# Kernel tuning notes

Hardware: AMD Instinct MI355X
Metric: run time of the kernel (lower is better)

## Reference

```python
import jax, jax.numpy as jnp
import numpy as np

# Fixed problem sizes (single FPN level, stride 8, 1280x1280 image)
N, A, C, H, W = 8, 1, 80, 160, 160
L = H * W * A
STRIDE = 8
IMG_SIZE = H * STRIDE
PRE_NMS_THRESH = 0.05
PRE_NMS_TOP_N = 1000
NMS_THRESH = 0.6
POST_TOP_N = 100
MIN_SIZE = 0.0
BBOX_XFORM_CLIP = float(np.log(1000.0 / 16.0))
TO_REMOVE = 1.0


def setup_inputs() -> dict:
    key = jax.random.key(0)
    k1, k2, k3 = jax.random.split(key, 3)
    box_regression = jax.random.normal(k1, (N, A * 4, H, W), jnp.float32)
    centerness = jax.random.normal(k2, (N, A, H, W), jnp.float32)
    box_cls = jax.random.normal(k3, (N, A * C, H, W), jnp.float32)
    # Anchor grid (one 8*stride/2-sized square anchor per location, shared across images)
    ys, xs = jnp.meshgrid(jnp.arange(H, dtype=jnp.float32), jnp.arange(W, dtype=jnp.float32), indexing="ij")
    cx = (xs.reshape(-1) + 0.5) * STRIDE
    cy = (ys.reshape(-1) + 0.5) * STRIDE
    half = 4.0 * STRIDE
    anchors = jnp.stack([cx - half, cy - half, cx + half, cy + half], axis=-1)  # [L,4] xyxy
    return {"box_regression": box_regression, "centerness": centerness, "box_cls": box_cls, "anchors": anchors}


def _flatten(x, c):
    # permute_and_flatten: [N, A*c, H, W] -> [N, H*W*A, c]
    return x.reshape(N, A, c, H, W).transpose(0, 3, 4, 1, 2).reshape(N, L, c)


def _decode(rel, anch):
    # ATSS BoxCoder.decode with weights (10,10,5,5)
    wx, wy, ww, wh = 10.0, 10.0, 5.0, 5.0
    widths = anch[:, 2] - anch[:, 0] + TO_REMOVE
    heights = anch[:, 3] - anch[:, 1] + TO_REMOVE
    ctr_x = anch[:, 0] + 0.5 * widths
    ctr_y = anch[:, 1] + 0.5 * heights
    dx = rel[:, 0] / wx
    dy = rel[:, 1] / wy
    dw = jnp.minimum(rel[:, 2] / ww, BBOX_XFORM_CLIP)
    dh = jnp.minimum(rel[:, 3] / wh, BBOX_XFORM_CLIP)
    pcx = dx * widths + ctr_x
    pcy = dy * heights + ctr_y
    pw = jnp.exp(dw) * widths
    ph = jnp.exp(dh) * heights
    return jnp.stack([pcx - 0.5 * (pw - TO_REMOVE), pcy - 0.5 * (ph - TO_REMOVE),
                      pcx + 0.5 * (pw - TO_REMOVE), pcy + 0.5 * (ph - TO_REMOVE)], axis=-1)


def _pairwise_iou(b):
    area = jnp.clip(b[:, 2] - b[:, 0], 0) * jnp.clip(b[:, 3] - b[:, 1], 0)
    lt = jnp.maximum(b[:, None, :2], b[None, :, :2])
    rb = jnp.minimum(b[:, None, 2:], b[None, :, 2:])
    wh = jnp.clip(rb - lt, 0)
    inter = wh[..., 0] * wh[..., 1]
    return inter / (area[:, None] + area[None, :] - inter + 1e-9)


def _per_image(scores, regression, cand, anchors):
    # scores [L,C] (already * centerness), cand [L,C] bool (thresholded BEFORE centerness)
    flat = jnp.where(cand, scores, -jnp.inf).reshape(-1)  # [L*C]
    vals, idx = jax.lax.top_k(flat, PRE_NMS_TOP_N)        # fixed-size pre-NMS topk
    loc = idx // C
    cls = idx % C + 1                                     # labels are 1-based
    valid = jnp.isfinite(vals)
    boxes = _decode(regression[loc], anchors[loc])
    x1 = jnp.clip(boxes[:, 0], 0.0, IMG_SIZE - 1.0)
    y1 = jnp.clip(boxes[:, 1], 0.0, IMG_SIZE - 1.0)
    x2 = jnp.clip(boxes[:, 2], 0.0, IMG_SIZE - 1.0)
    y2 = jnp.clip(boxes[:, 3], 0.0, IMG_SIZE - 1.0)
    boxes = jnp.stack([x1, y1, x2, y2], axis=-1)
    valid = valid & ((x2 - x1 + TO_REMOVE) >= MIN_SIZE) & ((y2 - y1 + TO_REMOVE) >= MIN_SIZE)
    sc = jnp.where(valid, jnp.sqrt(jnp.where(valid, vals, 1.0)), 0.0)
    # class-aware greedy NMS (boxlist_ml_nms): offset boxes by class so classes never overlap
    order = jnp.argsort(-jnp.where(valid, sc, -1.0))
    boxes, sc, cls, valid = boxes[order], sc[order], cls[order], valid[order]
    shifted = boxes + cls.astype(boxes.dtype)[:, None] * (4.0 * IMG_SIZE)
    iou = jax.lax.stop_gradient(_pairwise_iou(shifted))
    tri = jnp.triu(jnp.ones((PRE_NMS_TOP_N, PRE_NMS_TOP_N), bool), 1)
    iou = jnp.where(tri, iou, 0.0)

    def body(i, sup):
        keep_i = valid[i] & ~sup[i]
        return jnp.where(keep_i, sup | (iou[i] > NMS_THRESH), sup)

    sup = jax.lax.fori_loop(0, PRE_NMS_TOP_N, body, jnp.zeros(PRE_NMS_TOP_N, bool))
    keep = valid & ~sup
    fs = jnp.where(keep, sc, -1.0)
    topv, topi = jax.lax.top_k(fs, POST_TOP_N)            # fpn_post_nms_top_n cap
    ok = topv > 0
    out_boxes = jnp.where(ok[:, None], boxes[topi], 0.0)
    out_scores = jnp.where(ok, topv, 0.0)
    out_labels = jnp.where(ok, cls[topi], 0)
    dets = jnp.concatenate([out_boxes, out_scores[:, None]], axis=-1)  # [POST_TOP_N, 5]
    return dets, out_labels


def reference(box_regression, centerness, box_cls, anchors):
    cls_prob = jax.nn.sigmoid(_flatten(box_cls, C))                 # [N,L,C]
    ctr = jax.nn.sigmoid(_flatten(centerness, 1).reshape(N, L))     # [N,L]
    reg = _flatten(box_regression, 4)                               # [N,L,4]
    cand = cls_prob > PRE_NMS_THRESH                                # mask computed pre-centerness
    scores = cls_prob * ctr[:, :, None]
    dets, labels = jax.vmap(lambda s, r, c: _per_image(s, r, c, anchors))(scores, reg, cand)
    return dets, labels
```

## Files before the change

### kernel.cpp

```cpp
#include <hip/hip_runtime.h>
#include <cstdint>

static constexpr int NI   = 8;
static constexpr int CC   = 80;
static constexpr int LL   = 25600;
static constexpr int PRE_K  = 1000;
static constexpr int POST_K = 100;
static constexpr int HSIZE  = 2048;
static constexpr int CPCH   = 16;
static constexpr int NCH    = 5;
static constexpr int LPB    = 1024;
static constexpr int LBLK   = 25;
static constexpr int BPI    = NCH * LBLK;
static constexpr int CAPS   = 49152;
static constexpr int CAPFB  = 16384;
static constexpr int CAP2   = 8192;
static constexpr int BUFC   = 1024;
static constexpr float PRE_T = 0.05f;
static constexpr float NMS_T = 0.6f;
static constexpr float BSTAT = 0.65f;
static constexpr float XPRE  = 0.619f;
static constexpr uint32_t FBASE = 0x3F000000u;
static constexpr float CLIPV = 4.135166556742356f;
static constexpr float IMGM1 = 1279.0f;

__device__ __forceinline__ float sigm(float x) { return 1.0f / (1.0f + expf(-x)); }

__global__ __launch_bounds__(256) void k_scan(const float* __restrict__ cls,
                                              const float* __restrict__ ctr,
                                              uint32_t* __restrict__ cntS,
                                              uint32_t* __restrict__ ovf,
                                              unsigned long long* __restrict__ candS) {
    __shared__ unsigned long long sbuf[BUFC];
    __shared__ uint32_t s_cnt, s_base;
    const int t = threadIdx.x;
    if (t == 0) s_cnt = 0;
    __syncthreads();
    const int blk = blockIdx.x;
    const int n = blk / BPI, rem = blk % BPI, ch = rem / LBLK, lb = rem % LBLK;
    const int l0 = lb * LPB + t * 4;
    const uint32_t bstat = __float_as_uint(BSTAT);
    const float4 cr = *(const float4*)&ctr[(size_t)n * LL + l0];
    const float cv[4] = { sigm(cr.x), sigm(cr.y), sigm(cr.z), sigm(cr.w) };
    const float* base = cls + ((size_t)n * CC + ch * CPCH) * LL + l0;
#pragma unroll 1
    for (int cc0 = 0; cc0 < CPCH; cc0 += 4) {
        const float4 x0 = *(const float4*)&base[(size_t)(cc0 + 0) * LL];
        const float4 x1 = *(const float4*)&base[(size_t)(cc0 + 1) * LL];
        const float4 x2 = *(const float4*)&base[(size_t)(cc0 + 2) * LL];
        const float4 x3 = *(const float4*)&base[(size_t)(cc0 + 3) * LL];
        const float4 xs[4] = { x0, x1, x2, x3 };
#pragma unroll
        for (int u = 0; u < 4; ++u) {
            const float xv[4] = { xs[u].x, xs[u].y, xs[u].z, xs[u].w };
#pragma unroll
            for (int k = 0; k < 4; ++k) {
                if (xv[k] > XPRE) {
                    const float p = sigm(xv[k]);
                    if (p > PRE_T) {
                        const uint32_t bits = __float_as_uint(p * cv[k]);
                        if (bits >= bstat) {
                            uint32_t pos = atomicAdd(&s_cnt, 1u);
                            if (pos < (uint32_t)BUFC) {
                                uint32_t idx = (uint32_t)(l0 + k) * CC
                                             + (uint32_t)(ch * CPCH + cc0 + u);
                                sbuf[pos] = ((unsigned long long)bits << 32)
                                          | (uint32_t)(~idx);
                            }
                        }
                    }
                }
            }
        }
    }
    __syncthreads();
    if (t == 0) {
        s_base = atomicAdd(&cntS[n], s_cnt);
        if (s_cnt > (uint32_t)BUFC || s_base + s_cnt > (uint32_t)CAPS)
            atomicOr(&ovf[n], 1u);
    }
    __syncthreads();
    const uint32_t wr = min(s_cnt, (uint32_t)BUFC);
    const uint32_t b = s_base;
    if (b < (uint32_t)CAPS) {
        const uint32_t w = min(wr, (uint32_t)CAPS - b);
        for (uint32_t i = t; i < w; i += 256)
            candS[(size_t)n * CAPS + b + i] = sbuf[i];
    }
}

__global__ __launch_bounds__(256) void k_hist2(const unsigned long long* __restrict__ candS,
                                               const uint32_t* __restrict__ cntS,
                                               uint32_t* __restrict__ ghist2) {
    __shared__ uint32_t h[HSIZE];
    const int t = threadIdx.x;
    const int n = blockIdx.x >> 3, sub = blockIdx.x & 7;
    for (int i = t; i < HSIZE; i += 256) h[i] = 0u;
    __syncthreads();
    const uint32_t cnt = min(cntS[n], (uint32_t)CAPS);
    for (uint32_t i = (uint32_t)(sub * 256 + t); i < cnt; i += 2048) {
        const uint32_t bits = (uint32_t)(candS[(size_t)n * CAPS + i] >> 32);
        const uint32_t idx = min(2047u, (bits - FBASE) >> 12);
        atomicAdd(&h[idx], 1u);
    }
    __syncthreads();
    for (int b = t; b < HSIZE; b += 256)
        if (h[b]) atomicAdd(&ghist2[n * HSIZE + b], h[b]);
}

__global__ __launch_bounds__(256) void k_thresh2(const uint32_t* __restrict__ ghist2,
                                                 const uint32_t* __restrict__ cntS,
                                                 const uint32_t* __restrict__ ovf,
                                                 uint32_t* __restrict__ thr2,
                                                 uint32_t* __restrict__ listlen,
                                                 uint32_t* __restrict__ flag) {
    __shared__ uint32_t h[HSIZE];
    __shared__ uint32_t chunk[256];
    const int n = blockIdx.x, t = threadIdx.x;
    for (int b = t; b < HSIZE; b += 256) h[b] = ghist2[n * HSIZE + b];
    __syncthreads();
    uint32_t s = 0;
    for (int k = 0; k < 8; ++k) s += h[t * 8 + k];
    chunk[t] = s;
    __syncthreads();
    if (t == 0) {
        uint32_t cum = 0, nsel = 0;
        int T2 = -1;
        for (int c = 255; c >= 0 && T2 < 0; --c) {
            if (cum + chunk[c] >= (uint32_t)PRE_K) {
                for (int b = c * 8 + 7; b >= c * 8; --b) {
                    cum += h[b];
                    if (cum >= (uint32_t)PRE_K) { T2 = b; nsel = cum; break; }
                }
            } else cum += chunk[c];
        }
        const uint32_t tb = FBASE + ((uint32_t)max(T2, 0) << 12);
        thr2[n] = tb;
        listlen[n] = min(cntS[n], (uint32_t)CAPS);
        flag[n] = (T2 >= 0 && tb >= __float_as_uint(BSTAT) && !ovf[n] &&
                   nsel <= (uint32_t)CAP2) ? 1u : 0u;
    }
}

__global__ __launch_bounds__(256) void k_fbhist(const float* __restrict__ cls,
                                                const float* __restrict__ ctr,
                                                const uint32_t* __restrict__ flag,
                                                uint32_t* __restrict__ ghistC) {
    const int blk = blockIdx.x;
    const int n = blk / BPI;
    if (flag[n]) return;
    __shared__ uint32_t h[4][HSIZE];
    const int t = threadIdx.x;
    for (int i = t; i < 4 * HSIZE; i += 256) (&h[0][0])[i] = 0u;
    __syncthreads();
    const int rem = blk % BPI, ch = rem / LBLK, lb = rem % LBLK;
    const int l0 = lb * LPB + t * 4;
    const float4 cr = *(const float4*)&ctr[(size_t)n * LL + l0];
    const float cv[4] = { sigm(cr.x), sigm(cr.y), sigm(cr.z), sigm(cr.w) };
    uint32_t* hw = h[t >> 6];
    const float* base = cls + ((size_t)n * CC + ch * CPCH) * LL + l0;
#pragma unroll 1
    for (int cc = 0; cc < CPCH; ++cc) {
        const float4 x = *(const float4*)&base[(size_t)cc * LL];
        const float pv[4] = { sigm(x.x), sigm(x.y), sigm(x.z), sigm(x.w) };
#pragma unroll
        for (int k = 0; k < 4; ++k)
            if (pv[k] > PRE_T)
                atomicAdd(&hw[__float_as_uint(pv[k] * cv[k]) >> 19], 1u);
    }
    __syncthreads();
    for (int b = t; b < HSIZE; b += 256) {
        const uint32_t s = h[0][b] + h[1][b] + h[2][b] + h[3][b];
        if (s) atomicAdd(&ghistC[n * HSIZE + b], s);
    }
}

__global__ __launch_bounds__(256) void k_fbthresh(const uint32_t* __restrict__ ghistC,
                                                  const uint32_t* __restrict__ flag,
                                                  uint32_t* __restrict__ thr2) {
    const int n = blockIdx.x;
    if (flag[n]) return;
    __shared__ uint32_t h[HSIZE];
    __shared__ uint32_t chunk[256];
    const int t = threadIdx.x;
    for (int b = t; b < HSIZE; b += 256) h[b] = ghistC[n * HSIZE + b];
    __syncthreads();
    uint32_t s = 0;
    for (int k = 0; k < 8; ++k) s += h[t * 8 + k];
    chunk[t] = s;
    __syncthreads();
    if (t == 0) {
        uint32_t cum = 0;
        int T = 0;
        for (int c = 255; c >= 0; --c) {
            if (cum + chunk[c] >= (uint32_t)PRE_K) {
                for (int b = c * 8 + 7; b >= c * 8; --b) {
                    cum += h[b];
                    if (cum >= (uint32_t)PRE_K) { T = b; break; }
                }
                break;
            }
            cum += chunk[c];
        }
        thr2[n] = ((uint32_t)T) << 19;
    }
}

__global__ __launch_bounds__(256) void k_fbcollect(const float* __restrict__ cls,
                                                   const float* __restrict__ ctr,
                                                   const uint32_t* __restrict__ flag,
                                                   const uint32_t* __restrict__ thr2,
                                                   uint32_t* __restrict__ cntFB,
                                                   unsigned long long* __restrict__ candFB) {
    const int blk = blockIdx.x;
    const int n = blk / BPI;
    if (flag[n]) return;
    const int t = threadIdx.x;
    const int rem = blk % BPI, ch = rem / LBLK, lb = rem % LBLK;
    const int l0 = lb * LPB + t * 4;
    const uint32_t th = thr2[n];
    const float4 cr = *(const float4*)&ctr[(size_t)n * LL + l0];
    const float cv[4] = { sigm(cr.x), sigm(cr.y), sigm(cr.z), sigm(cr.w) };
    const float* base = cls + ((size_t)n * CC + ch * CPCH) * LL + l0;
#pragma unroll 1
    for (int cc = 0; cc < CPCH; ++cc) {
        const float4 x = *(const float4*)&base[(size_t)cc * LL];
        const float pv[4] = { sigm(x.x), sigm(x.y), sigm(x.z), sigm(x.w) };
#pragma unroll
        for (int k = 0; k < 4; ++k) {
            if (pv[k] > PRE_T) {
                const uint32_t bits = __float_as_uint(pv[k] * cv[k]);
                if (bits >= th) {
                    uint32_t pos = atomicAdd(&cntFB[n], 1u);
                    if (pos < (uint32_t)CAPFB) {
                        uint32_t idx = (uint32_t)(l0 + k) * CC + (uint32_t)(ch * CPCH + cc);
                        candFB[(size_t)n * CAPFB + pos] =
                            ((unsigned long long)bits << 32) | (uint32_t)(~idx);
                    }
                }
            }
        }
    }
}

__global__ __launch_bounds__(1024) void k_sortnms(const unsigned long long* __restrict__ candS,
                                                  const uint32_t* __restrict__ listlen,
                                                  const unsigned long long* __restrict__ candFB,
                                                  const uint32_t* __restrict__ cntFB,
                                                  unsigned long long* __restrict__ cand2,
                                                  const uint32_t* __restrict__ thr2,
                                                  const uint32_t* __restrict__ flag,
                                                  const float* __restrict__ reg,
                                                  const float* __restrict__ anch,
                                                  float* __restrict__ out) {
    __shared__ unsigned long long buf[2048];
    __shared__ float bx0[PRE_K], bx1[PRE_K], bx2[PRE_K], bx3[PRE_K];
    __shared__ float ar[PRE_K], scv[PRE_K];
    __shared__ int clsA[PRE_K], sup[PRE_K];
    __shared__ uint32_t s_cnt;
    __shared__ int s_kept;
    __shared__ int s_list[POST_K];
    const int n = blockIdx.x, t = threadIdx.x;
    if (t == 0) { s_cnt = 0; s_kept = 0; }
    __syncthreads();

    const bool fp = (flag[n] != 0);
    const unsigned long long* src = fp ? (candS + (size_t)n * CAPS)
                                       : (candFB + (size_t)n * CAPFB);
    const uint32_t len = fp ? listlen[n] : min(cntFB[n], (uint32_t)CAPFB);
    const unsigned long long Tkey = ((unsigned long long)thr2[n]) << 32;
    for (uint32_t gi = t; gi < len; gi += 1024) {
        const unsigned long long key = src[gi];
        if (key >= Tkey) {
            uint32_t pos = atomicAdd(&s_cnt, 1u);
            if (pos < (uint32_t)CAP2) cand2[(size_t)n * CAP2 + pos] = key;
        }
    }
    __syncthreads();
    const uint32_t M = min(s_cnt, (uint32_t)CAP2);

    buf[t]        = ((uint32_t)t < M)          ? cand2[(size_t)n * CAP2 + t]        : 0ULL;
    buf[1024 + t] = ((uint32_t)(1024 + t) < M) ? cand2[(size_t)n * CAP2 + 1024 + t] : 0ULL;
    for (uint32_t s = 0;;) {
        for (int k = 2; k <= 2048; k <<= 1) {
            for (int j = k >> 1; j > 0; j >>= 1) {
                __syncthreads();
#pragma unroll
                for (int u = 0; u < 2; ++u) {
                    const int i = t + u * 1024;
                    const int ixj = i ^ j;
                    if (ixj > i) {
                        const unsigned long long a = buf[i], b = buf[ixj];
                        const bool desc = ((i & k) == 0);
                        if (desc ? (a < b) : (a > b)) { buf[i] = b; buf[ixj] = a; }
                    }
                }
            }
        }
        __syncthreads();
        s = (s == 0) ? 2048 : s + 1024;
        if (s >= M) break;
        buf[1024 + t] = (s + t < M) ? cand2[(size_t)n * CAP2 + s + t] : 0ULL;
        __syncthreads();
    }

    if (t < PRE_K) {
        const unsigned long long key = buf[t];
        if (key == 0ULL) {
            sup[t] = 2; clsA[t] = -1;
            bx0[t] = bx1[t] = bx2[t] = bx3[t] = 0.0f; ar[t] = 0.0f; scv[t] = 0.0f;
        } else {
            const uint32_t bits = (uint32_t)(key >> 32);
            const uint32_t idx = ~(uint32_t)key;
            const int l = (int)(idx / (uint32_t)CC);
            const int c = (int)(idx % (uint32_t)CC);
            const float4 a = *(const float4*)&anch[l * 4];
            const float r0 = reg[((size_t)n * 4 + 0) * LL + l];
            const float r1 = reg[((size_t)n * 4 + 1) * LL + l];
            const float r2 = reg[((size_t)n * 4 + 2) * LL + l];
            const float r3 = reg[((size_t)n * 4 + 3) * LL + l];
            const float w  = a.z - a.x + 1.0f;
            const float h  = a.w - a.y + 1.0f;
            const float cx = a.x + 0.5f * w;
            const float cy = a.y + 0.5f * h;
            const float dx = r0 / 10.0f, dy = r1 / 10.0f;
            const float dw = fminf(r2 / 5.0f, CLIPV), dh = fminf(r3 / 5.0f, CLIPV);
            const float pcx = dx * w + cx, pcy = dy * h + cy;
            const float pw = expf(dw) * w, ph = expf(dh) * h;
            float x1 = pcx - 0.5f * (pw - 1.0f);
            float y1 = pcy - 0.5f * (ph - 1.0f);
            float x2 = pcx + 0.5f * (pw - 1.0f);
            float y2 = pcy + 0.5f * (ph - 1.0f);
            x1 = fminf(fmaxf(x1, 0.0f), IMGM1);
            y1 = fminf(fmaxf(y1, 0.0f), IMGM1);
            x2 = fminf(fmaxf(x2, 0.0f), IMGM1);
            y2 = fminf(fmaxf(y2, 0.0f), IMGM1);
            bx0[t] = x1; bx1[t] = y1; bx2[t] = x2; bx3[t] = y2;
            ar[t] = fmaxf(x2 - x1, 0.0f) * fmaxf(y2 - y1, 0.0f);
            scv[t] = sqrtf(__uint_as_float(bits));
            clsA[t] = c + 1;
            sup[t] = 0;
        }
    }
    __syncthreads();

    for (int i = 0; i < PRE_K; ++i) {
        if (s_kept >= POST_K) break;
        if (sup[i] == 0) {
            if (t == 0) s_list[s_kept] = i;
            if (t > i && t < PRE_K && sup[t] == 0 && clsA[t] == clsA[i]) {
                const float xx1 = fmaxf(bx0[i], bx0[t]);
                const float yy1 = fmaxf(bx1[i], bx1[t]);
                const float xx2 = fminf(bx2[i], bx2[t]);
                const float yy2 = fminf(bx3[i], bx3[t]);
                const float iw = fmaxf(xx2 - xx1, 0.0f);
                const float ih = fmaxf(yy2 - yy1, 0.0f);
                const float inter = iw * ih;
                const float iou = inter / (ar[i] + ar[t] - inter + 1e-9f);
                if (iou > NMS_T) sup[t] = 1;
            }
            if (t == 0) s_kept = s_kept + 1;
        }
        __syncthreads();
    }
    __syncthreads();

    if (t < POST_K) {
        float o0 = 0.f, o1 = 0.f, o2 = 0.f, o3 = 0.f, o4 = 0.f, lab = 0.f;
        if (t < s_kept) {
            const int i = s_list[t];
            o0 = bx0[i]; o1 = bx1[i]; o2 = bx2[i]; o3 = bx3[i];
            o4 = scv[i]; lab = (float)clsA[i];
        }
        float* dets = out + (size_t)(n * POST_K + t) * 5;
        dets[0] = o0; dets[1] = o1; dets[2] = o2; dets[3] = o3; dets[4] = o4;
        out[(size_t)NI * POST_K * 5 + (size_t)n * POST_K + t] = lab;
    }
}

extern "C" void kernel_launch(void* const* d_in, const int* in_sizes, int n_in,
                              void* d_out, int out_size, void* d_ws, size_t ws_size,
                              hipStream_t stream) {
    const float* reg  = (const float*)d_in[0];
    const float* ctr  = (const float*)d_in[1];
    const float* cls  = (const float*)d_in[2];
    const float* anch = (const float*)d_in[3];
    float* out = (float*)d_out;

    char* ws = (char*)d_ws;
    size_t off = 0;
    uint32_t* ghist2 = (uint32_t*)(ws + off); off += (size_t)NI * HSIZE * 4;
    uint32_t* ghistC = (uint32_t*)(ws + off); off += (size_t)NI * HSIZE * 4;
    uint32_t* cntS   = (uint32_t*)(ws + off); off += 32;
    uint32_t* ovf    = (uint32_t*)(ws + off); off += 32;
    uint32_t* cntFB  = (uint32_t*)(ws + off); off += 32;
    const size_t zbytes = off;
    uint32_t* thr2    = (uint32_t*)(ws + off); off += 32;
    uint32_t* listlen = (uint32_t*)(ws + off); off += 32;
    uint32_t* flg     = (uint32_t*)(ws + off); off += 32;
    unsigned long long* candS  = (unsigned long long*)(ws + off); off += (size_t)NI * CAPS * 8;
    unsigned long long* candFB = (unsigned long long*)(ws + off); off += (size_t)NI * CAPFB * 8;
    unsigned long long* cand2  = (unsigned long long*)(ws + off); off += (size_t)NI * CAP2 * 8;

    hipMemsetAsync(ghist2, 0, zbytes, stream);
    k_scan     <<<NI * BPI, 256, 0, stream>>>(cls, ctr, cntS, ovf, candS);
    k_hist2    <<<NI * 8,   256, 0, stream>>>(candS, cntS, ghist2);
    k_thresh2  <<<NI,       256, 0, stream>>>(ghist2, cntS, ovf, thr2, listlen, flg);
    k_fbhist   <<<NI * BPI, 256, 0, stream>>>(cls, ctr, flg, ghistC);
    k_fbthresh <<<NI,       256, 0, stream>>>(ghistC, flg, thr2);
    k_fbcollect<<<NI * BPI, 256, 0, stream>>>(cls, ctr, flg, thr2, cntFB, candFB);
    k_sortnms  <<<NI,      1024, 0, stream>>>(candS, listlen, candFB, cntFB, cand2,
                                              thr2, flg, reg, anch, out);
}
```

Measured before the change: 227.7 us.

## Replace bitonic sort + serial NMS with rank-select and parallel IoU bitmask NMS

Replaces the single-block bitonic sort with a rank-by-counting selection that writes the top-1000 boxes to global SoA arrays. The serial, barrier-per-iteration NMS becomes a precomputed IoU bitmask spread over 16 blocks per image, followed by a single-wavefront greedy scan using shuffles. It also merges the histogram and threshold kernels, and halves the channels per scan block with a fully unrolled load. The counting rank costs O(M^2) per image and adds extra launches.

```diff
diff --git a/kernel.cpp b/kernel.cpp
--- a/kernel.cpp
+++ b/kernel.cpp
@@ -1,37 +1,26 @@
 #include <hip/hip_runtime.h>
 #include <cstdint>
 
-static constexpr int NI   = 8;
-static constexpr int CC   = 80;
-static constexpr int LL   = 25600;
-static constexpr int PRE_K  = 1000;
-static constexpr int POST_K = 100;
-static constexpr int HSIZE  = 2048;
-static constexpr int CPCH   = 16;
-static constexpr int NCH    = 5;
-static constexpr int LPB    = 1024;
-static constexpr int LBLK   = 25;
-static constexpr int BPI    = NCH * LBLK;
-static constexpr int CAPS   = 49152;
-static constexpr int CAPFB  = 16384;
-static constexpr int CAP2   = 8192;
-static constexpr int BUFC   = 1024;
-static constexpr float PRE_T = 0.05f;
-static constexpr float NMS_T = 0.6f;
-static constexpr float BSTAT = 0.65f;
-static constexpr float XPRE  = 0.619f;
-static constexpr uint32_t FBASE = 0x3F000000u;
-static constexpr float CLIPV = 4.135166556742356f;
-static constexpr float IMGM1 = 1279.0f;
-
-__device__ __forceinline__ float sigm(float x) { return 1.0f / (1.0f + expf(-x)); }
+static constexpr int NI=8, CC=80, LL=25600, PRE_K=1000, POST_K=100;
+static constexpr int HSIZE=2048;
+static constexpr int CPCH=8, NCH=10, LPB=1024, LBLK=25, BPI=NCH*LBLK;
+static constexpr int BUFC=768;
+static constexpr int CAPS=49152;
+static constexpr int CAPFB=8192;
+static constexpr int CAP2=8192;
+static constexpr float NMS_T=0.6f, BSTAT=0.65f, XPRE=0.619f;
+static constexpr uint32_t FBASE=0x3F000000u;
+static constexpr float CLIPV=4.135166556742356f, IMGM1=1279.0f;
+typedef unsigned long long u64;
+
+__device__ __forceinline__ float sigm(float x){ return 1.0f/(1.0f+expf(-x)); }
 
 __global__ __launch_bounds__(256) void k_scan(const float* __restrict__ cls,
                                               const float* __restrict__ ctr,
                                               uint32_t* __restrict__ cntS,
                                               uint32_t* __restrict__ ovf,
-                                              unsigned long long* __restrict__ candS) {
-    __shared__ unsigned long long sbuf[BUFC];
+                                              u64* __restrict__ candS) {
+    __shared__ u64 sbuf[BUFC];
     __shared__ uint32_t s_cnt, s_base;
     const int t = threadIdx.x;
     if (t == 0) s_cnt = 0;
@@ -43,31 +32,27 @@
     const float4 cr = *(const float4*)&ctr[(size_t)n * LL + l0];
     const float cv[4] = { sigm(cr.x), sigm(cr.y), sigm(cr.z), sigm(cr.w) };
     const float* base = cls + ((size_t)n * CC + ch * CPCH) * LL + l0;
-#pragma unroll 1
-    for (int cc0 = 0; cc0 < CPCH; cc0 += 4) {
-        const float4 x0 = *(const float4*)&base[(size_t)(cc0 + 0) * LL];
-        const float4 x1 = *(const float4*)&base[(size_t)(cc0 + 1) * LL];
-        const float4 x2 = *(const float4*)&base[(size_t)(cc0 + 2) * LL];
-        const float4 x3 = *(const float4*)&base[(size_t)(cc0 + 3) * LL];
-        const float4 xs[4] = { x0, x1, x2, x3 };
+    const float4 x0 = *(const float4*)&base[(size_t)0 * LL];
+    const float4 x1 = *(const float4*)&base[(size_t)1 * LL];
+    const float4 x2 = *(const float4*)&base[(size_t)2 * LL];
+    const float4 x3 = *(const float4*)&base[(size_t)3 * LL];
+    const float4 x4 = *(const float4*)&base[(size_t)4 * LL];
+    const float4 x5 = *(const float4*)&base[(size_t)5 * LL];
+    const float4 x6 = *(const float4*)&base[(size_t)6 * LL];
+    const float4 x7 = *(const float4*)&base[(size_t)7 * LL];
+    const float4 xs[8] = { x0, x1, x2, x3, x4, x5, x6, x7 };
 #pragma unroll
-        for (int u = 0; u < 4; ++u) {
-            const float xv[4] = { xs[u].x, xs[u].y, xs[u].z, xs[u].w };
+    for (int u = 0; u < CPCH; ++u) {
+        const float xv[4] = { xs[u].x, xs[u].y, xs[u].z, xs[u].w };
 #pragma unroll
-            for (int k = 0; k < 4; ++k) {
-                if (xv[k] > XPRE) {
-                    const float p = sigm(xv[k]);
-                    if (p > PRE_T) {
-                        const uint32_t bits = __float_as_uint(p * cv[k]);
-                        if (bits >= bstat) {
-                            uint32_t pos = atomicAdd(&s_cnt, 1u);
-                            if (pos < (uint32_t)BUFC) {
-                                uint32_t idx = (uint32_t)(l0 + k) * CC
-                                             + (uint32_t)(ch * CPCH + cc0 + u);
-                                sbuf[pos] = ((unsigned long long)bits << 32)
-                                          | (uint32_t)(~idx);
-                            }
-                        }
+        for (int k = 0; k < 4; ++k) {
+            if (xv[k] > XPRE) {
+                const uint32_t bits = __float_as_uint(sigm(xv[k]) * cv[k]);
+                if (bits >= bstat) {
+                    uint32_t pos = atomicAdd(&s_cnt, 1u);
+                    if (pos < (uint32_t)BUFC) {
+                        uint32_t idx = (uint32_t)(l0 + k) * CC + (uint32_t)(ch * CPCH + u);
+                        sbuf[pos] = ((u64)bits << 32) | (uint32_t)(~idx);
                     }
                 }
             }
@@ -89,35 +74,22 @@
     }
 }
 
-__global__ __launch_bounds__(256) void k_hist2(const unsigned long long* __restrict__ candS,
-                                               const uint32_t* __restrict__ cntS,
-                                               uint32_t* __restrict__ ghist2) {
-    __shared__ uint32_t h[HSIZE];
-    const int t = threadIdx.x;
-    const int n = blockIdx.x >> 3, sub = blockIdx.x & 7;
-    for (int i = t; i < HSIZE; i += 256) h[i] = 0u;
-    __syncthreads();
-    const uint32_t cnt = min(cntS[n], (uint32_t)CAPS);
-    for (uint32_t i = (uint32_t)(sub * 256 + t); i < cnt; i += 2048) {
-        const uint32_t bits = (uint32_t)(candS[(size_t)n * CAPS + i] >> 32);
-        const uint32_t idx = min(2047u, (bits - FBASE) >> 12);
-        atomicAdd(&h[idx], 1u);
-    }
-    __syncthreads();
-    for (int b = t; b < HSIZE; b += 256)
-        if (h[b]) atomicAdd(&ghist2[n * HSIZE + b], h[b]);
-}
-
-__global__ __launch_bounds__(256) void k_thresh2(const uint32_t* __restrict__ ghist2,
-                                                 const uint32_t* __restrict__ cntS,
-                                                 const uint32_t* __restrict__ ovf,
-                                                 uint32_t* __restrict__ thr2,
-                                                 uint32_t* __restrict__ listlen,
-                                                 uint32_t* __restrict__ flag) {
+__global__ __launch_bounds__(256) void k_thresh(const u64* __restrict__ candS,
+                                                const uint32_t* __restrict__ cntS,
+                                                const uint32_t* __restrict__ ovf,
+                                                uint32_t* __restrict__ thr2,
+                                                uint32_t* __restrict__ listlen,
+                                                uint32_t* __restrict__ flag) {
     __shared__ uint32_t h[HSIZE];
     __shared__ uint32_t chunk[256];
     const int n = blockIdx.x, t = threadIdx.x;
-    for (int b = t; b < HSIZE; b += 256) h[b] = ghist2[n * HSIZE + b];
+    for (int i = t; i < HSIZE; i += 256) h[i] = 0u;
+    __syncthreads();
+    const uint32_t cnt = min(cntS[n], (uint32_t)CAPS);
+    for (uint32_t i = t; i < cnt; i += 256) {
+        const uint32_t bits = (uint32_t)(candS[(size_t)n * CAPS + i] >> 32);
+        atomicAdd(&h[min(2047u, (bits - FBASE) >> 12)], 1u);
+    }
     __syncthreads();
     uint32_t s = 0;
     for (int k = 0; k < 8; ++k) s += h[t * 8 + k];
@@ -136,7 +108,7 @@
         }
         const uint32_t tb = FBASE + ((uint32_t)max(T2, 0) << 12);
         thr2[n] = tb;
-        listlen[n] = min(cntS[n], (uint32_t)CAPS);
+        listlen[n] = cnt;
         flag[n] = (T2 >= 0 && tb >= __float_as_uint(BSTAT) && !ovf[n] &&
                    nsel <= (uint32_t)CAP2) ? 1u : 0u;
     }
@@ -165,7 +137,7 @@
         const float pv[4] = { sigm(x.x), sigm(x.y), sigm(x.z), sigm(x.w) };
 #pragma unroll
         for (int k = 0; k < 4; ++k)
-            if (pv[k] > PRE_T)
+            if (pv[k] > 0.05f)
                 atomicAdd(&hw[__float_as_uint(pv[k] * cv[k]) >> 19], 1u);
     }
     __syncthreads();
@@ -211,7 +183,7 @@
                                                    const uint32_t* __restrict__ flag,
                                                    const uint32_t* __restrict__ thr2,
                                                    uint32_t* __restrict__ cntFB,
-                                                   unsigned long long* __restrict__ candFB) {
+                                                   u64* __restrict__ candFB) {
     const int blk = blockIdx.x;
     const int n = blk / BPI;
     if (flag[n]) return;
@@ -228,14 +200,14 @@
         const float pv[4] = { sigm(x.x), sigm(x.y), sigm(x.z), sigm(x.w) };
 #pragma unroll
         for (int k = 0; k < 4; ++k) {
-            if (pv[k] > PRE_T) {
+            if (pv[k] > 0.05f) {
                 const uint32_t bits = __float_as_uint(pv[k] * cv[k]);
                 if (bits >= th) {
                     uint32_t pos = atomicAdd(&cntFB[n], 1u);
                     if (pos < (uint32_t)CAPFB) {
                         uint32_t idx = (uint32_t)(l0 + k) * CC + (uint32_t)(ch * CPCH + cc);
                         candFB[(size_t)n * CAPFB + pos] =
-                            ((unsigned long long)bits << 32) | (uint32_t)(~idx);
+                            ((u64)bits << 32) | (uint32_t)(~idx);
                     }
                 }
             }
@@ -243,82 +215,55 @@
     }
 }
 
-__global__ __launch_bounds__(1024) void k_sortnms(const unsigned long long* __restrict__ candS,
-                                                  const uint32_t* __restrict__ listlen,
-                                                  const unsigned long long* __restrict__ candFB,
-                                                  const uint32_t* __restrict__ cntFB,
-                                                  unsigned long long* __restrict__ cand2,
-                                                  const uint32_t* __restrict__ thr2,
-                                                  const uint32_t* __restrict__ flag,
-                                                  const float* __restrict__ reg,
-                                                  const float* __restrict__ anch,
-                                                  float* __restrict__ out) {
-    __shared__ unsigned long long buf[2048];
-    __shared__ float bx0[PRE_K], bx1[PRE_K], bx2[PRE_K], bx3[PRE_K];
-    __shared__ float ar[PRE_K], scv[PRE_K];
-    __shared__ int clsA[PRE_K], sup[PRE_K];
+__global__ __launch_bounds__(1024) void k_prep(const u64* __restrict__ candS,
+                                               const uint32_t* __restrict__ listlen,
+                                               const u64* __restrict__ candFB,
+                                               const uint32_t* __restrict__ cntFB,
+                                               const uint32_t* __restrict__ thr2,
+                                               const uint32_t* __restrict__ flag,
+                                               const float* __restrict__ reg,
+                                               const float* __restrict__ anch,
+                                               float* __restrict__ X1, float* __restrict__ Y1,
+                                               float* __restrict__ X2, float* __restrict__ Y2,
+                                               float* __restrict__ AR, float* __restrict__ SC,
+                                               int* __restrict__ CL) {
+    __shared__ u64 list[CAP2];
     __shared__ uint32_t s_cnt;
-    __shared__ int s_kept;
-    __shared__ int s_list[POST_K];
     const int n = blockIdx.x, t = threadIdx.x;
-    if (t == 0) { s_cnt = 0; s_kept = 0; }
-    __syncthreads();
-
+    if (t == 0) s_cnt = 0;
+    __syncthreads();
     const bool fp = (flag[n] != 0);
-    const unsigned long long* src = fp ? (candS + (size_t)n * CAPS)
-                                       : (candFB + (size_t)n * CAPFB);
+    const u64* src = fp ? (candS + (size_t)n * CAPS) : (candFB + (size_t)n * CAPFB);
     const uint32_t len = fp ? listlen[n] : min(cntFB[n], (uint32_t)CAPFB);
-    const unsigned long long Tkey = ((unsigned long long)thr2[n]) << 32;
+    const u64 Tkey = ((u64)thr2[n]) << 32;
     for (uint32_t gi = t; gi < len; gi += 1024) {
-        const unsigned long long key = src[gi];
+        const u64 key = src[gi];
         if (key >= Tkey) {
             uint32_t pos = atomicAdd(&s_cnt, 1u);
-            if (pos < (uint32_t)CAP2) cand2[(size_t)n * CAP2 + pos] = key;
-        }
+            if (pos < (uint32_t)CAP2) list[pos] = key;
+        }
+    }
+    const int gb = n * 1024;
+    for (int r = t; r < PRE_K; r += 1024) {
+        X1[gb+r]=0.f; Y1[gb+r]=0.f; X2[gb+r]=0.f; Y2[gb+r]=0.f;
+        AR[gb+r]=0.f; SC[gb+r]=0.f; CL[gb+r]=0;
     }
     __syncthreads();
     const uint32_t M = min(s_cnt, (uint32_t)CAP2);
-
-    buf[t]        = ((uint32_t)t < M)          ? cand2[(size_t)n * CAP2 + t]        : 0ULL;
-    buf[1024 + t] = ((uint32_t)(1024 + t) < M) ? cand2[(size_t)n * CAP2 + 1024 + t] : 0ULL;
-    for (uint32_t s = 0;;) {
-        for (int k = 2; k <= 2048; k <<= 1) {
-            for (int j = k >> 1; j > 0; j >>= 1) {
-                __syncthreads();
-#pragma unroll
-                for (int u = 0; u < 2; ++u) {
-                    const int i = t + u * 1024;
-                    const int ixj = i ^ j;
-                    if (ixj > i) {
-                        const unsigned long long a = buf[i], b = buf[ixj];
-                        const bool desc = ((i & k) == 0);
-                        if (desc ? (a < b) : (a > b)) { buf[i] = b; buf[ixj] = a; }
-                    }
-                }
-            }
-        }
-        __syncthreads();
-        s = (s == 0) ? 2048 : s + 1024;
-        if (s >= M) break;
-        buf[1024 + t] = (s + t < M) ? cand2[(size_t)n * CAP2 + s + t] : 0ULL;
-        __syncthreads();
-    }
-
-    if (t < PRE_K) {
-        const unsigned long long key = buf[t];
-        if (key == 0ULL) {
-            sup[t] = 2; clsA[t] = -1;
-            bx0[t] = bx1[t] = bx2[t] = bx3[t] = 0.0f; ar[t] = 0.0f; scv[t] = 0.0f;
-        } else {
+    for (uint32_t ci = t; ci < M; ci += 1024) {
+        const u64 key = list[ci];
+        uint32_t rank = 0;
+        for (uint32_t j = 0; j < M; ++j) rank += (list[j] > key);
+        if (rank < (uint32_t)PRE_K) {
             const uint32_t bits = (uint32_t)(key >> 32);
             const uint32_t idx = ~(uint32_t)key;
             const int l = (int)(idx / (uint32_t)CC);
             const int c = (int)(idx % (uint32_t)CC);
             const float4 a = *(const float4*)&anch[l * 4];
-            const float r0 = reg[((size_t)n * 4 + 0) * LL + l];
-            const float r1 = reg[((size_t)n * 4 + 1) * LL + l];
-            const float r2 = reg[((size_t)n * 4 + 2) * LL + l];
-            const float r3 = reg[((size_t)n * 4 + 3) * LL + l];
+            const float r0 = reg[((size_t)n*4+0)*LL + l];
+            const float r1 = reg[((size_t)n*4+1)*LL + l];
+            const float r2 = reg[((size_t)n*4+2)*LL + l];
+            const float r3 = reg[((size_t)n*4+3)*LL + l];
             const float w  = a.z - a.x + 1.0f;
             const float h  = a.w - a.y + 1.0f;
             const float cx = a.x + 0.5f * w;
@@ -335,45 +280,104 @@
             y1 = fminf(fmaxf(y1, 0.0f), IMGM1);
             x2 = fminf(fmaxf(x2, 0.0f), IMGM1);
             y2 = fminf(fmaxf(y2, 0.0f), IMGM1);
-            bx0[t] = x1; bx1[t] = y1; bx2[t] = x2; bx3[t] = y2;
-            ar[t] = fmaxf(x2 - x1, 0.0f) * fmaxf(y2 - y1, 0.0f);
-            scv[t] = sqrtf(__uint_as_float(bits));
-            clsA[t] = c + 1;
-            sup[t] = 0;
-        }
-    }
-    __syncthreads();
-
-    for (int i = 0; i < PRE_K; ++i) {
-        if (s_kept >= POST_K) break;
-        if (sup[i] == 0) {
-            if (t == 0) s_list[s_kept] = i;
-            if (t > i && t < PRE_K && sup[t] == 0 && clsA[t] == clsA[i]) {
-                const float xx1 = fmaxf(bx0[i], bx0[t]);
-                const float yy1 = fmaxf(bx1[i], bx1[t]);
-                const float xx2 = fminf(bx2[i], bx2[t]);
-                const float yy2 = fminf(bx3[i], bx3[t]);
-                const float iw = fmaxf(xx2 - xx1, 0.0f);
-                const float ih = fmaxf(yy2 - yy1, 0.0f);
-                const float inter = iw * ih;
-                const float iou = inter / (ar[i] + ar[t] - inter + 1e-9f);
-                if (iou > NMS_T) sup[t] = 1;
+            X1[gb+rank]=x1; Y1[gb+rank]=y1; X2[gb+rank]=x2; Y2[gb+rank]=y2;
+            AR[gb+rank]=fmaxf(x2-x1,0.0f)*fmaxf(y2-y1,0.0f);
+            SC[gb+rank]=sqrtf(__uint_as_float(bits));
+            CL[gb+rank]=c+1;
+        }
+    }
+}
+
+__global__ __launch_bounds__(256) void k_mask(const float* __restrict__ X1, const float* __restrict__ Y1,
+                                              const float* __restrict__ X2, const float* __restrict__ Y2,
+                                              const float* __restrict__ AR, const int* __restrict__ CL,
+                                              u64* __restrict__ mask) {
+    __shared__ float lx1[PRE_K], ly1[PRE_K], lx2[PRE_K], ly2[PRE_K], lar[PRE_K];
+    __shared__ int lcl[PRE_K];
+    const int n = blockIdx.x >> 4, tile = blockIdx.x & 15, t = threadIdx.x;
+    const int gb = n * 1024;
+    for (int i = t; i < PRE_K; i += 256) {
+        lx1[i]=X1[gb+i]; ly1[i]=Y1[gb+i]; lx2[i]=X2[gb+i]; ly2[i]=Y2[gb+i];
+        lar[i]=AR[gb+i]; lcl[i]=CL[gb+i];
+    }
+    __syncthreads();
+#pragma unroll
+    for (int u = 0; u < 4; ++u) {
+        const int task = t + 256 * u;
+        const int row = task >> 4, word = task & 15;
+        const int gr = tile * 64 + row;
+        u64 bits = 0ull;
+        if (gr < PRE_K) {
+            const int rcl = lcl[gr];
+            if (rcl != 0) {
+                const float rx1=lx1[gr], ry1=ly1[gr], rx2=lx2[gr], ry2=ly2[gr], rar=lar[gr];
+                const int jb = word * 64;
+                for (int jj = 0; jj < 64; ++jj) {
+                    const int j = jb + jj;
+                    if (j > gr && j < PRE_K && lcl[j] == rcl) {
+                        const float xx1 = fmaxf(rx1, lx1[j]);
+                        const float yy1 = fmaxf(ry1, ly1[j]);
+                        const float xx2 = fminf(rx2, lx2[j]);
+                        const float yy2 = fminf(ry2, ly2[j]);
+                        const float iw = fmaxf(xx2 - xx1, 0.0f);
+                        const float ih = fmaxf(yy2 - yy1, 0.0f);
+                        const float inter = iw * ih;
+                        const float iou = inter / (rar + lar[j] - inter + 1e-9f);
+                        if (iou > NMS_T) bits |= (1ull << jj);
+                    }
+                }
             }
-            if (t == 0) s_kept = s_kept + 1;
-        }
-        __syncthreads();
-    }
-    __syncthreads();
-
+        }
+        mask[((size_t)(gb + ((gr < 1024) ? gr : 0)) ) * 16 + word] = bits;
+    }
+}
+
+__global__ __launch_bounds__(256) void k_final(const u64* __restrict__ mask,
+                                               const float* __restrict__ X1, const float* __restrict__ Y1,
+                                               const float* __restrict__ X2, const float* __restrict__ Y2,
+                                               const float* __restrict__ SC, const int* __restrict__ CL,
+                                               float* __restrict__ out) {
+    __shared__ u64 lmask[256 * 16];
+    __shared__ int lcl[PRE_K];
+    __shared__ int s_keep[POST_K];
+    __shared__ int s_kept;
+    const int n = blockIdx.x, t = threadIdx.x;
+    const int gb = n * 1024;
+    for (int i = t; i < 256 * 16; i += 256) lmask[i] = mask[(size_t)gb * 16 + i];
+    for (int i = t; i < PRE_K; i += 256) lcl[i] = CL[gb + i];
+    __syncthreads();
+    if (t < 64) {
+        u64 sup = 0ull;
+        int kept = 0;
+        for (int i = 0; i < PRE_K; ++i) {
+            const int w = i >> 6, b = i & 63;
+            const unsigned int lo = __shfl((unsigned int)(sup & 0xffffffffu), w);
+            const unsigned int hi = __shfl((unsigned int)(sup >> 32), w);
+            const u64 supw = ((u64)hi << 32) | lo;
+            const bool keep = (lcl[i] != 0) && !((supw >> b) & 1ull);
+            if (keep) {
+                if (t == 0) s_keep[kept] = i;
+                ++kept;
+                if (kept >= POST_K) break;
+                if (t < 16) {
+                    const u64 row = (i < 256) ? lmask[i * 16 + t]
+                                              : mask[(size_t)(gb + i) * 16 + t];
+                    sup |= row;
+                }
+            }
+        }
+        if (t == 0) s_kept = kept;
+    }
+    __syncthreads();
     if (t < POST_K) {
-        float o0 = 0.f, o1 = 0.f, o2 = 0.f, o3 = 0.f, o4 = 0.f, lab = 0.f;
+        float o0=0.f, o1=0.f, o2=0.f, o3=0.f, o4=0.f, lab=0.f;
         if (t < s_kept) {
-            const int i = s_list[t];
-            o0 = bx0[i]; o1 = bx1[i]; o2 = bx2[i]; o3 = bx3[i];
-            o4 = scv[i]; lab = (float)clsA[i];
+            const int i = s_keep[t];
+            o0=X1[gb+i]; o1=Y1[gb+i]; o2=X2[gb+i]; o3=Y2[gb+i];
+            o4=SC[gb+i]; lab=(float)CL[gb+i];
         }
         float* dets = out + (size_t)(n * POST_K + t) * 5;
-        dets[0] = o0; dets[1] = o1; dets[2] = o2; dets[3] = o3; dets[4] = o4;
+        dets[0]=o0; dets[1]=o1; dets[2]=o2; dets[3]=o3; dets[4]=o4;
         out[(size_t)NI * POST_K * 5 + (size_t)n * POST_K + t] = lab;
     }
 }
@@ -389,26 +393,33 @@
 
     char* ws = (char*)d_ws;
     size_t off = 0;
-    uint32_t* ghist2 = (uint32_t*)(ws + off); off += (size_t)NI * HSIZE * 4;
-    uint32_t* ghistC = (uint32_t*)(ws + off); off += (size_t)NI * HSIZE * 4;
     uint32_t* cntS   = (uint32_t*)(ws + off); off += 32;
     uint32_t* ovf    = (uint32_t*)(ws + off); off += 32;
     uint32_t* cntFB  = (uint32_t*)(ws + off); off += 32;
+    uint32_t* ghistC = (uint32_t*)(ws + off); off += (size_t)NI * HSIZE * 4;
     const size_t zbytes = off;
     uint32_t* thr2    = (uint32_t*)(ws + off); off += 32;
     uint32_t* listlen = (uint32_t*)(ws + off); off += 32;
     uint32_t* flg     = (uint32_t*)(ws + off); off += 32;
-    unsigned long long* candS  = (unsigned long long*)(ws + off); off += (size_t)NI * CAPS * 8;
-    unsigned long long* candFB = (unsigned long long*)(ws + off); off += (size_t)NI * CAPFB * 8;
-    unsigned long long* cand2  = (unsigned long long*)(ws + off); off += (size_t)NI * CAP2 * 8;
-
-    hipMemsetAsync(ghist2, 0, zbytes, stream);
+    u64* candS  = (u64*)(ws + off); off += (size_t)NI * CAPS * 8;
+    u64* candFB = (u64*)(ws + off); off += (size_t)NI * CAPFB * 8;
+    float* X1 = (float*)(ws + off); off += NI * 1024 * 4;
+    float* Y1 = (float*)(ws + off); off += NI * 1024 * 4;
+    float* X2 = (float*)(ws + off); off += NI * 1024 * 4;
+    float* Y2 = (float*)(ws + off); off += NI * 1024 * 4;
+    float* AR = (float*)(ws + off); off += NI * 1024 * 4;
+    float* SC = (float*)(ws + off); off += NI * 1024 * 4;
+    int*   CL = (int*)(ws + off);   off += NI * 1024 * 4;
+    u64* mask = (u64*)(ws + off);   off += (size_t)NI * 1024 * 16 * 8;
+
+    hipMemsetAsync(cntS, 0, zbytes, stream);
     k_scan     <<<NI * BPI, 256, 0, stream>>>(cls, ctr, cntS, ovf, candS);
-    k_hist2    <<<NI * 8,   256, 0, stream>>>(candS, cntS, ghist2);
-    k_thresh2  <<<NI,       256, 0, stream>>>(ghist2, cntS, ovf, thr2, listlen, flg);
+    k_thresh   <<<NI,       256, 0, stream>>>(candS, cntS, ovf, thr2, listlen, flg);
     k_fbhist   <<<NI * BPI, 256, 0, stream>>>(cls, ctr, flg, ghistC);
     k_fbthresh <<<NI,       256, 0, stream>>>(ghistC, flg, thr2);
     k_fbcollect<<<NI * BPI, 256, 0, stream>>>(cls, ctr, flg, thr2, cntFB, candFB);
-    k_sortnms  <<<NI,      1024, 0, stream>>>(candS, listlen, candFB, cntFB, cand2,
-                                              thr2, flg, reg, anch, out);
-}
+    k_prep     <<<NI,      1024, 0, stream>>>(candS, listlen, candFB, cntFB, thr2, flg,
+                                              reg, anch, X1, Y1, X2, Y2, AR, SC, CL);
+    k_mask     <<<NI * 16,  256, 0, stream>>>(X1, Y1, X2, Y2, AR, CL, mask);
+    k_final    <<<NI,       256, 0, stream>>>(mask, X1, Y1, X2, Y2, SC, CL, out);
+}
```

Measured after the change: 270.7 us. +18.8%, slower.
